# Optimization experiments

Hardware: AMD Instinct MI355X
Metric: run time of the kernel (lower is better)

## Reference

```python
import jax, jax.numpy as jnp
import numpy as np

LN_EPS = 1e-5

def _layernorm(x, g, b):
    mu = jnp.mean(x, axis=-1, keepdims=True)
    var = jnp.mean(jnp.square(x - mu), axis=-1, keepdims=True)
    return (x - mu) * jax.lax.rsqrt(var + LN_EPS) * g + b

def setup_inputs() -> dict:
    key = jax.random.key(0)
    ks = jax.random.split(key, 8)
    b, n, h = 2, 64, 32
    edge_in = 1            # edge_dim(0) + 1
    mid = 128
    nc_in, nc_out, num_freq = 32, 32, 5   # degrees 2,2 -> to_order=5
    out_dim = nc_out * nc_in * num_freq   # 5120, rearranged '(o i f)'
    d_in = d_out = 5
    s1 = 1.0 / np.sqrt(edge_in)
    s2 = 1.0 / np.sqrt(mid)
    return {
        "feat": jax.random.normal(ks[0], (b, n, h, edge_in), jnp.float32),
        "basis": jax.random.normal(ks[1], (b, n, h, 1, d_out, 1, d_in, num_freq), jnp.float32),
        "W1": jax.random.normal(ks[2], (edge_in, mid), jnp.float32) * s1,
        "b1": jnp.zeros((mid,), jnp.float32),
        "g1": jnp.ones((mid,), jnp.float32),
        "beta1": jnp.zeros((mid,), jnp.float32),
        "W2": jax.random.normal(ks[3], (mid, mid), jnp.float32) * s2,
        "b2": jnp.zeros((mid,), jnp.float32),
        "g2": jnp.ones((mid,), jnp.float32),
        "beta2": jnp.zeros((mid,), jnp.float32),
        "W3": jax.random.normal(ks[4], (mid, out_dim), jnp.float32) * s2,
        "b3": jnp.zeros((out_dim,), jnp.float32),
    }

def reference(feat, basis, W1, b1, g1, beta1, W2, b2, g2, beta2, W3, b3):
    nc_out, nc_in, num_freq = 32, 32, 5
    # RadialFunc MLP: Linear -> LN -> ReLU -> Linear -> LN -> ReLU -> Linear
    x = jax.nn.relu(_layernorm(feat @ W1 + b1, g1, beta1))
    x = jax.nn.relu(_layernorm(x @ W2 + b2, g2, beta2))
    y = x @ W3 + b3                                   # (b,n,h, o*i*f)
    bb, nn_, hh = y.shape[0], y.shape[1], y.shape[2]
    R = y.reshape(bb, nn_, hh, nc_out, nc_in, num_freq)  # '(o i f)' split order
    B = basis[:, :, :, 0, :, 0, :, :]                 # (b,n,h,d_out,d_in,f)
    # fused broadcast-multiply-reduce over frequency axis f
    out = jnp.einsum('bnhoif,bnhdmf->bnhodim', R, B)  # (b,n,h,o,d_out,i,d_in)
    d_out, d_in = B.shape[3], B.shape[4]
    return out.reshape(bb, nn_, hh, nc_out * d_out, nc_in * d_in)
```

## Files before the change

### kernel.cpp

```cpp
#include <hip/hip_runtime.h>

#define LN_EPS 1e-5f

typedef __attribute__((ext_vector_type(8)))  short bf16x8;
typedef __attribute__((ext_vector_type(16))) float floatx16;

static __device__ __forceinline__ unsigned short f2bf(float x) {
    union { float f; unsigned u; } v; v.f = x;
    unsigned r = v.u + 0x7FFFu + ((v.u >> 16) & 1u);
    return (unsigned short)(r >> 16);
}

__global__ __launch_bounds__(256) void k1_mlp(
    const float* __restrict__ feat,
    const float* __restrict__ W1, const float* __restrict__ b1,
    const float* __restrict__ g1, const float* __restrict__ be1,
    const float* __restrict__ W2, const float* __restrict__ b2,
    const float* __restrict__ g2, const float* __restrict__ be2,
    float* __restrict__ x2out)
{
    const int ty = threadIdx.x >> 7;
    const int j  = threadIdx.x & 127;
    const int row = blockIdx.x * 2 + ty;

    __shared__ float sx1[2][128];
    __shared__ float sred[2][2][2];

    const float f = feat[row];
    float v = fmaf(f, W1[j], b1[j]);

    float s = v, q = v * v;
    #pragma unroll
    for (int off = 32; off > 0; off >>= 1) {
        s += __shfl_down(s, off);
        q += __shfl_down(q, off);
    }
    const int wir = j >> 6;
    if ((j & 63) == 0) { sred[ty][wir][0] = s; sred[ty][wir][1] = q; }
    __syncthreads();
    float sum = sred[ty][0][0] + sred[ty][1][0];
    float sq  = sred[ty][0][1] + sred[ty][1][1];
    float mu  = sum * (1.0f / 128.0f);
    float var = fmaf(-mu, mu, sq * (1.0f / 128.0f));
    float x1  = fmaf((v - mu) * rsqrtf(var + LN_EPS), g1[j], be1[j]);
    x1 = fmaxf(x1, 0.0f);
    sx1[ty][j] = x1;
    __syncthreads();

    float a = b2[j];
    #pragma unroll 8
    for (int k = 0; k < 128; ++k)
        a = fmaf(sx1[ty][k], W2[k * 128 + j], a);

    s = a; q = a * a;
    #pragma unroll
    for (int off = 32; off > 0; off >>= 1) {
        s += __shfl_down(s, off);
        q += __shfl_down(q, off);
    }
    if ((j & 63) == 0) { sred[ty][wir][0] = s; sred[ty][wir][1] = q; }
    __syncthreads();
    sum = sred[ty][0][0] + sred[ty][1][0];
    sq  = sred[ty][0][1] + sred[ty][1][1];
    mu  = sum * (1.0f / 128.0f);
    var = fmaf(-mu, mu, sq * (1.0f / 128.0f));
    float x2v = fmaf((a - mu) * rsqrtf(var + LN_EPS), g2[j], be2[j]);
    x2v = fmaxf(x2v, 0.0f);
    x2out[row * 128 + j] = x2v;
}

__global__ __launch_bounds__(256) void k_repack_x(
    const float* __restrict__ x2, unsigned int* __restrict__ A)
{
    const int g = blockIdx.x * 256 + threadIdx.x;
    const int L = g & 63;
    const int s = (g >> 6) & 7;
    const int R = g >> 9;
    const int row = R * 32 + (L & 31);
    const int kb  = s * 16 + (L >> 5) * 8;
    const float4* src = (const float4*)(x2 + (size_t)row * 128 + kb);
    float4 a = src[0], b = src[1];
    uint4 w;
    w.x = f2bf(a.x) | ((unsigned)f2bf(a.y) << 16);
    w.y = f2bf(a.z) | ((unsigned)f2bf(a.w) << 16);
    w.z = f2bf(b.x) | ((unsigned)f2bf(b.y) << 16);
    w.w = f2bf(b.z) | ((unsigned)f2bf(b.w) << 16);
    ((uint4*)A)[g] = w;
}

__global__ __launch_bounds__(256) void k_repack_w(
    const float* __restrict__ W3, unsigned int* __restrict__ B)
{
    const int g = blockIdx.x * 256 + threadIdx.x;
    const int L = g & 63;
    const int s = (g >> 6) & 7;
    const int t = g >> 9;
    const int n  = t * 32 + (L & 31);
    const int kb = s * 16 + (L >> 5) * 8;
    unsigned short o[8];
    #pragma unroll
    for (int j = 0; j < 8; ++j)
        o[j] = f2bf(W3[(size_t)(kb + j) * 5120 + n]);
    uint4 w;
    w.x = o[0] | ((unsigned)o[1] << 16);
    w.y = o[2] | ((unsigned)o[3] << 16);
    w.z = o[4] | ((unsigned)o[5] << 16);
    w.w = o[6] | ((unsigned)o[7] << 16);
    ((uint4*)B)[g] = w;
}

__global__ __launch_bounds__(256) void k_gemm(
    const unsigned int* __restrict__ Abf, const unsigned int* __restrict__ Bbf,
    const float* __restrict__ b3, float* __restrict__ Y)
{
    const int lane = threadIdx.x & 63;
    const int w    = threadIdx.x >> 6;
    const int R    = blockIdx.x;
    const int cb   = blockIdx.y;
    const int t0   = cb * 20 + w * 5;

    floatx16 acc[5];
    #pragma unroll
    for (int tt = 0; tt < 5; ++tt) acc[tt] = (floatx16)0.0f;

    const uint4* Ap = (const uint4*)Abf + (size_t)R * 512 + lane;
    const uint4* Bp = (const uint4*)Bbf + (size_t)t0 * 512 + lane;

    #pragma unroll
    for (int s = 0; s < 8; ++s) {
        bf16x8 a = *(const bf16x8*)(Ap + s * 64);
        #pragma unroll
        for (int tt = 0; tt < 5; ++tt) {
            bf16x8 b = *(const bf16x8*)(Bp + (size_t)tt * 512 + s * 64);
            acc[tt] = __builtin_amdgcn_mfma_f32_32x32x16_bf16(a, b, acc[tt], 0, 0, 0);
        }
    }

    const int m_hi = 4 * (lane >> 5);
    const int nl   = lane & 31;
    float* yb = Y + (size_t)R * 32 * 5120;
    #pragma unroll
    for (int tt = 0; tt < 5; ++tt) {
        const int n = (t0 + tt) * 32 + nl;
        const float bias = b3[n];
        #pragma unroll
        for (int reg = 0; reg < 16; ++reg) {
            const int m = (reg & 3) + 8 * (reg >> 2) + m_hi;
            yb[(size_t)m * 5120 + n] = acc[tt][reg] + bias;
        }
    }
}

__global__ __launch_bounds__(256) void k_einsum(
    const float* __restrict__ Y, const float* __restrict__ basis,
    float* __restrict__ out)
{
    const int tid = threadIdx.x;
    const int tx  = tid & 31;
    const int ty  = tid >> 5;
    const int row0 = blockIdx.x * 32;
    const int p0   = blockIdx.y * 128;

    __shared__ float sB[32 * 125];
    for (int idx = tid; idx < 32 * 125; idx += 256)
        sB[idx] = basis[(size_t)row0 * 125 + idx];
    __syncthreads();

    float acc[4][20];
    #pragma unroll
    for (int r = 0; r < 4; ++r) {
        const float4* yp = (const float4*)(Y + (size_t)(row0 + ty * 4 + r) * 5120
                                             + p0 * 5 + tx * 20);
        float4 q0 = yp[0], q1 = yp[1], q2 = yp[2], q3 = yp[3], q4 = yp[4];
        acc[r][0]=q0.x;  acc[r][1]=q0.y;  acc[r][2]=q0.z;  acc[r][3]=q0.w;
        acc[r][4]=q1.x;  acc[r][5]=q1.y;  acc[r][6]=q1.z;  acc[r][7]=q1.w;
        acc[r][8]=q2.x;  acc[r][9]=q2.y;  acc[r][10]=q2.z; acc[r][11]=q2.w;
        acc[r][12]=q3.x; acc[r][13]=q3.y; acc[r][14]=q3.z; acc[r][15]=q3.w;
        acc[r][16]=q4.x; acc[r][17]=q4.y; acc[r][18]=q4.z; acc[r][19]=q4.w;
    }

    const int pb = p0 + tx * 4;
    const int o  = pb >> 5;
    const int i0 = pb & 31;

    #pragma unroll
    for (int rs = 0; rs < 4; ++rs) {
        const int rl = ty * 4 + rs;
        float* orow = out + (size_t)(row0 + rl) * 25600 + (size_t)o * 800 + i0 * 5;
        const float* Br = sB + rl * 125;
        #pragma unroll
        for (int d = 0; d < 5; ++d) {
            float Bv[25];
            #pragma unroll
            for (int qq = 0; qq < 25; ++qq) Bv[qq] = Br[d * 25 + qq];
            float vv[20];
            #pragma unroll
            for (int p = 0; p < 4; ++p) {
                #pragma unroll
                for (int m = 0; m < 5; ++m) {
                    float t = acc[rs][p * 5 + 0] * Bv[m * 5 + 0];
                    t = fmaf(acc[rs][p * 5 + 1], Bv[m * 5 + 1], t);
                    t = fmaf(acc[rs][p * 5 + 2], Bv[m * 5 + 2], t);
                    t = fmaf(acc[rs][p * 5 + 3], Bv[m * 5 + 3], t);
                    t = fmaf(acc[rs][p * 5 + 4], Bv[m * 5 + 4], t);
                    vv[p * 5 + m] = t;
                }
            }
            float4* dst = (float4*)(orow + d * 160);
            dst[0] = make_float4(vv[0],  vv[1],  vv[2],  vv[3]);
            dst[1] = make_float4(vv[4],  vv[5],  vv[6],  vv[7]);
            dst[2] = make_float4(vv[8],  vv[9],  vv[10], vv[11]);
            dst[3] = make_float4(vv[12], vv[13], vv[14], vv[15]);
            dst[4] = make_float4(vv[16], vv[17], vv[18], vv[19]);
        }
    }
}

extern "C" void kernel_launch(void* const* d_in, const int* in_sizes, int n_in,
                              void* d_out, int out_size, void* d_ws, size_t ws_size,
                              hipStream_t stream)
{
    const float* feat  = (const float*)d_in[0];
    const float* basis = (const float*)d_in[1];
    const float* W1    = (const float*)d_in[2];
    const float* b1    = (const float*)d_in[3];
    const float* g1    = (const float*)d_in[4];
    const float* be1   = (const float*)d_in[5];
    const float* W2    = (const float*)d_in[6];
    const float* b2    = (const float*)d_in[7];
    const float* g2    = (const float*)d_in[8];
    const float* be2   = (const float*)d_in[9];
    const float* W3    = (const float*)d_in[10];
    const float* b3    = (const float*)d_in[11];

    float* out = (float*)d_out;

    char* ws = (char*)d_ws;
    float*        x2  = (float*)(ws);
    unsigned int* Abf = (unsigned int*)(ws + 2097152);
    unsigned int* Bbf = (unsigned int*)(ws + 3145728);
    float*        Yt  = (float*)(ws + 4456448);

    const int rows = 4096;

    k1_mlp<<<rows / 2, 256, 0, stream>>>(feat, W1, b1, g1, be1, W2, b2, g2, be2, x2);
    k_repack_x<<<256, 256, 0, stream>>>(x2, Abf);
    k_repack_w<<<320, 256, 0, stream>>>(W3, Bbf);

    dim3 ggrid(rows / 32, 8);
    k_gemm<<<ggrid, 256, 0, stream>>>(Abf, Bbf, b3, Yt);

    dim3 egrid(rows / 32, 8);
    k_einsum<<<egrid, 256, 0, stream>>>(Yt, basis, out);
}
```

Baseline: 558.2 us.

## Fuse GEMM with einsum epilogue and write bf16 MFMA layout from MLP kernel

The MLP kernel now writes its output directly as bf16 in the MFMA-packed layout, which removes the separate x repack kernel and its fp32 intermediate. The W3 GEMM and the basis einsum are merged into one kernel. Accumulators plus bias are staged through shared memory in two phases and contracted with the basis held in shared memory, so the 80 MB fp32 Y intermediate is no longer written to or read back from global memory. The cost is larger LDS use and extra barriers per block, and the output store pattern and bank conflicts on the shared staging buffer may change.

After: 536.0 us. -4.0%, faster.

```diff
diff --git a/kernel.cpp b/kernel.cpp
--- a/kernel.cpp
+++ b/kernel.cpp
@@ -17,7 +17,7 @@
     const float* __restrict__ g1, const float* __restrict__ be1,
     const float* __restrict__ W2, const float* __restrict__ b2,
     const float* __restrict__ g2, const float* __restrict__ be2,
-    float* __restrict__ x2out)
+    unsigned short* __restrict__ Abf)
 {
     const int ty = threadIdx.x >> 7;
     const int j  = threadIdx.x & 127;
@@ -66,26 +66,12 @@
     var = fmaf(-mu, mu, sq * (1.0f / 128.0f));
     float x2v = fmaf((a - mu) * rsqrtf(var + LN_EPS), g2[j], be2[j]);
     x2v = fmaxf(x2v, 0.0f);
-    x2out[row * 128 + j] = x2v;
-}
-
-__global__ __launch_bounds__(256) void k_repack_x(
-    const float* __restrict__ x2, unsigned int* __restrict__ A)
-{
-    const int g = blockIdx.x * 256 + threadIdx.x;
-    const int L = g & 63;
-    const int s = (g >> 6) & 7;
-    const int R = g >> 9;
-    const int row = R * 32 + (L & 31);
-    const int kb  = s * 16 + (L >> 5) * 8;
-    const float4* src = (const float4*)(x2 + (size_t)row * 128 + kb);
-    float4 a = src[0], b = src[1];
-    uint4 w;
-    w.x = f2bf(a.x) | ((unsigned)f2bf(a.y) << 16);
-    w.y = f2bf(a.z) | ((unsigned)f2bf(a.w) << 16);
-    w.z = f2bf(b.x) | ((unsigned)f2bf(b.y) << 16);
-    w.w = f2bf(b.z) | ((unsigned)f2bf(b.w) << 16);
-    ((uint4*)A)[g] = w;
+
+    const int s4 = j >> 4;
+    const int hi = (j >> 3) & 1;
+    const int jj = j & 7;
+    const int g  = ((row >> 5) * 8 + s4) * 64 + (row & 31) + 32 * hi;
+    Abf[(size_t)g * 8 + jj] = f2bf(x2v);
 }
 
 __global__ __launch_bounds__(256) void k_repack_w(
@@ -109,15 +95,23 @@
     ((uint4*)B)[g] = w;
 }
 
-__global__ __launch_bounds__(256) void k_gemm(
+__global__ __launch_bounds__(256) void k_fused(
     const unsigned int* __restrict__ Abf, const unsigned int* __restrict__ Bbf,
-    const float* __restrict__ b3, float* __restrict__ Y)
-{
-    const int lane = threadIdx.x & 63;
-    const int w    = threadIdx.x >> 6;
+    const float* __restrict__ b3, const float* __restrict__ basis,
+    float* __restrict__ out)
+{
+    const int tid  = threadIdx.x;
+    const int lane = tid & 63;
+    const int w    = tid >> 6;
     const int R    = blockIdx.x;
     const int cb   = blockIdx.y;
     const int t0   = cb * 20 + w * 5;
+
+    __shared__ float sY[2][32][160];
+    __shared__ float sB[32 * 125];
+
+    for (int idx = tid; idx < 32 * 125; idx += 256)
+        sB[idx] = basis[(size_t)R * (32 * 125) + idx];
 
     floatx16 acc[5];
     #pragma unroll
@@ -138,81 +132,72 @@
 
     const int m_hi = 4 * (lane >> 5);
     const int nl   = lane & 31;
-    float* yb = Y + (size_t)R * 32 * 5120;
-    #pragma unroll
-    for (int tt = 0; tt < 5; ++tt) {
-        const int n = (t0 + tt) * 32 + nl;
-        const float bias = b3[n];
-        #pragma unroll
-        for (int reg = 0; reg < 16; ++reg) {
-            const int m = (reg & 3) + 8 * (reg >> 2) + m_hi;
-            yb[(size_t)m * 5120 + n] = acc[tt][reg] + bias;
-        }
-    }
-}
-
-__global__ __launch_bounds__(256) void k_einsum(
-    const float* __restrict__ Y, const float* __restrict__ basis,
-    float* __restrict__ out)
-{
-    const int tid = threadIdx.x;
-    const int tx  = tid & 31;
-    const int ty  = tid >> 5;
-    const int row0 = blockIdx.x * 32;
-    const int p0   = blockIdx.y * 128;
-
-    __shared__ float sB[32 * 125];
-    for (int idx = tid; idx < 32 * 125; idx += 256)
-        sB[idx] = basis[(size_t)row0 * 125 + idx];
-    __syncthreads();
-
-    float acc[4][20];
-    #pragma unroll
-    for (int r = 0; r < 4; ++r) {
-        const float4* yp = (const float4*)(Y + (size_t)(row0 + ty * 4 + r) * 5120
-                                             + p0 * 5 + tx * 20);
-        float4 q0 = yp[0], q1 = yp[1], q2 = yp[2], q3 = yp[3], q4 = yp[4];
-        acc[r][0]=q0.x;  acc[r][1]=q0.y;  acc[r][2]=q0.z;  acc[r][3]=q0.w;
-        acc[r][4]=q1.x;  acc[r][5]=q1.y;  acc[r][6]=q1.z;  acc[r][7]=q1.w;
-        acc[r][8]=q2.x;  acc[r][9]=q2.y;  acc[r][10]=q2.z; acc[r][11]=q2.w;
-        acc[r][12]=q3.x; acc[r][13]=q3.y; acc[r][14]=q3.z; acc[r][15]=q3.w;
-        acc[r][16]=q4.x; acc[r][17]=q4.y; acc[r][18]=q4.z; acc[r][19]=q4.w;
-    }
-
-    const int pb = p0 + tx * 4;
-    const int o  = pb >> 5;
-    const int i0 = pb & 31;
-
-    #pragma unroll
-    for (int rs = 0; rs < 4; ++rs) {
-        const int rl = ty * 4 + rs;
-        float* orow = out + (size_t)(row0 + rl) * 25600 + (size_t)o * 800 + i0 * 5;
-        const float* Br = sB + rl * 125;
-        #pragma unroll
-        for (int d = 0; d < 5; ++d) {
-            float Bv[25];
+    float bias[5];
+    #pragma unroll
+    for (int tt = 0; tt < 5; ++tt) bias[tt] = b3[(t0 + tt) * 32 + nl];
+
+    const int l128 = tid & 127;
+    const int oh   = tid >> 7;
+    const int r0   = (l128 >> 3) * 2;
+    const int i0   = (l128 & 7) * 4;
+
+    #pragma unroll
+    for (int ph = 0; ph < 2; ++ph) {
+        if ((w >> 1) == ph) {
             #pragma unroll
-            for (int qq = 0; qq < 25; ++qq) Bv[qq] = Br[d * 25 + qq];
-            float vv[20];
-            #pragma unroll
-            for (int p = 0; p < 4; ++p) {
+            for (int tt = 0; tt < 5; ++tt) {
                 #pragma unroll
-                for (int m = 0; m < 5; ++m) {
-                    float t = acc[rs][p * 5 + 0] * Bv[m * 5 + 0];
-                    t = fmaf(acc[rs][p * 5 + 1], Bv[m * 5 + 1], t);
-                    t = fmaf(acc[rs][p * 5 + 2], Bv[m * 5 + 2], t);
-                    t = fmaf(acc[rs][p * 5 + 3], Bv[m * 5 + 3], t);
-                    t = fmaf(acc[rs][p * 5 + 4], Bv[m * 5 + 4], t);
-                    vv[p * 5 + m] = t;
+                for (int reg = 0; reg < 16; ++reg) {
+                    const int m = (reg & 3) + 8 * (reg >> 2) + m_hi;
+                    sY[w & 1][m][tt * 32 + nl] = acc[tt][reg] + bias[tt];
                 }
             }
-            float4* dst = (float4*)(orow + d * 160);
-            dst[0] = make_float4(vv[0],  vv[1],  vv[2],  vv[3]);
-            dst[1] = make_float4(vv[4],  vv[5],  vv[6],  vv[7]);
-            dst[2] = make_float4(vv[8],  vv[9],  vv[10], vv[11]);
-            dst[3] = make_float4(vv[12], vv[13], vv[14], vv[15]);
-            dst[4] = make_float4(vv[16], vv[17], vv[18], vv[19]);
         }
+        __syncthreads();
+
+        const int o = cb * 4 + ph * 2 + oh;
+        #pragma unroll
+        for (int rr = 0; rr < 2; ++rr) {
+            const int row = r0 + rr;
+            const float4* yp = (const float4*)(&sY[oh][row][i0 * 5]);
+            float4 q0 = yp[0], q1 = yp[1], q2 = yp[2], q3 = yp[3], q4 = yp[4];
+            float y[20];
+            y[0]=q0.x;  y[1]=q0.y;  y[2]=q0.z;  y[3]=q0.w;
+            y[4]=q1.x;  y[5]=q1.y;  y[6]=q1.z;  y[7]=q1.w;
+            y[8]=q2.x;  y[9]=q2.y;  y[10]=q2.z; y[11]=q2.w;
+            y[12]=q3.x; y[13]=q3.y; y[14]=q3.z; y[15]=q3.w;
+            y[16]=q4.x; y[17]=q4.y; y[18]=q4.z; y[19]=q4.w;
+
+            const float* Br = sB + row * 125;
+            float* orow = out + (size_t)(R * 32 + row) * 25600
+                              + (size_t)o * 800 + i0 * 5;
+            #pragma unroll
+            for (int d = 0; d < 5; ++d) {
+                float Bv[25];
+                #pragma unroll
+                for (int qq = 0; qq < 25; ++qq) Bv[qq] = Br[d * 25 + qq];
+                float vv[20];
+                #pragma unroll
+                for (int p = 0; p < 4; ++p) {
+                    #pragma unroll
+                    for (int m = 0; m < 5; ++m) {
+                        float t = y[p * 5 + 0] * Bv[m * 5 + 0];
+                        t = fmaf(y[p * 5 + 1], Bv[m * 5 + 1], t);
+                        t = fmaf(y[p * 5 + 2], Bv[m * 5 + 2], t);
+                        t = fmaf(y[p * 5 + 3], Bv[m * 5 + 3], t);
+                        t = fmaf(y[p * 5 + 4], Bv[m * 5 + 4], t);
+                        vv[p * 5 + m] = t;
+                    }
+                }
+                float4* dst = (float4*)(orow + d * 160);
+                dst[0] = make_float4(vv[0],  vv[1],  vv[2],  vv[3]);
+                dst[1] = make_float4(vv[4],  vv[5],  vv[6],  vv[7]);
+                dst[2] = make_float4(vv[8],  vv[9],  vv[10], vv[11]);
+                dst[3] = make_float4(vv[12], vv[13], vv[14], vv[15]);
+                dst[4] = make_float4(vv[16], vv[17], vv[18], vv[19]);
+            }
+        }
+        __syncthreads();
     }
 }
 
@@ -236,20 +221,14 @@
     float* out = (float*)d_out;
 
     char* ws = (char*)d_ws;
-    float*        x2  = (float*)(ws);
-    unsigned int* Abf = (unsigned int*)(ws + 2097152);
-    unsigned int* Bbf = (unsigned int*)(ws + 3145728);
-    float*        Yt  = (float*)(ws + 4456448);
+    unsigned short* Abf = (unsigned short*)(ws);
+    unsigned int*   Bbf = (unsigned int*)(ws + 1048576);
 
     const int rows = 4096;
 
-    k1_mlp<<<rows / 2, 256, 0, stream>>>(feat, W1, b1, g1, be1, W2, b2, g2, be2, x2);
-    k_repack_x<<<256, 256, 0, stream>>>(x2, Abf);
-    k_repack_w<<<320, 256, 0, stream>>>(W3, Bbf);
-
-    dim3 ggrid(rows / 32, 8);
-    k_gemm<<<ggrid, 256, 0, stream>>>(Abf, Bbf, b3, Yt);
-
-    dim3 egrid(rows / 32, 8);
-    k_einsum<<<egrid, 256, 0, stream>>>(Yt, basis, out);
-}
+    k1_mlp<<<rows / 2, 256, 0, stream>>>(feat, W1, b1, g1, be1, W2, b2, g2, be2, Abf);
+    k_repack_w<<<320, 256, 0, stream>>>(W3, (unsigned int*)Bbf);
+
+    dim3 fgrid(rows / 32, 8);
+    k_fused<<<fgrid, 256, 0, stream>>>((const unsigned int*)Abf, Bbf, b3, basis, out);
+}
```
